# Kernel tuning notes

Measured on AMD Instinct MI355X. Metric: run time of the kernel, lower is better.

The kernel has to match this reference:

```python
import jax, jax.numpy as jnp
import numpy as np

T, B, V, E, H, L = 128, 32, 50000, 512, 512, 2


def _lstm_layer(x, h0, c0, Wih, Whh, bih, bhh):
    # x: [T, B, in]; torch gate order i, f, g, o
    def step(carry, xt):
        h, c = carry
        gates = xt @ Wih.T + bih + h @ Whh.T + bhh  # [B, 4H]
        i, f, g, o = jnp.split(gates, 4, axis=-1)
        c = jax.nn.sigmoid(f) * c + jax.nn.sigmoid(i) * jnp.tanh(g)
        h = jax.nn.sigmoid(o) * jnp.tanh(c)
        return (h, c), h
    (h, c), ys = jax.lax.scan(step, (h0, c0), x)
    return ys, h, c


def setup_inputs() -> dict:
    key = jax.random.key(0)
    ks = jax.random.split(key, 12)
    s = 0.02
    return {
        'word': jax.random.randint(ks[0], (B,), 0, V),
        'seq': jax.random.randint(ks[1], (T, B), 0, V),
        'emb': jax.random.normal(ks[2], (V, E), jnp.float32) * s,
        'w2h_W': jax.random.normal(ks[3], (H, E), jnp.float32) * s,
        'w2h_b': jnp.zeros((H,), jnp.float32),
        'Wih0': jax.random.normal(ks[4], (4 * H, E), jnp.float32) * s,
        'Whh0': jax.random.normal(ks[5], (4 * H, H), jnp.float32) * s,
        'bih0': jnp.zeros((4 * H,), jnp.float32),
        'bhh0': jnp.zeros((4 * H,), jnp.float32),
        'Wih1': jax.random.normal(ks[6], (4 * H, H), jnp.float32) * s,
        'Whh1': jax.random.normal(ks[7], (4 * H, H), jnp.float32) * s,
        'bih1': jnp.zeros((4 * H,), jnp.float32),
        'bhh1': jnp.zeros((4 * H,), jnp.float32),
        'dec_W': jax.random.normal(ks[8], (V, H), jnp.float32) * s,
        'dec_b': jnp.zeros((V,), jnp.float32),
    }


def reference(word, seq, emb, w2h_W, w2h_b, Wih0, Whh0, bih0, bhh0,
              Wih1, Whh1, bih1, bhh1, dec_W, dec_b):
    word_emb = emb[word]                       # [B, E]
    seq_emb = emb[seq]                         # [T, B, E] (dropouts are 0/eval)
    # init_hidden: c0 = word2hidden(word_emb) expanded to all layers, h0 = 0
    c0 = word_emb @ w2h_W.T + w2h_b            # [B, H]
    h0 = jnp.zeros_like(c0)
    # 2-layer LSTM; stepping all layers per timestep == running layers sequentially
    y0, h_f0, c_f0 = _lstm_layer(seq_emb, h0, c0, Wih0, Whh0, bih0, bhh0)
    y1, h_f1, c_f1 = _lstm_layer(y0, h0, c0, Wih1, Whh1, bih1, bhh1)
    out = y1.reshape(T * B, H)                 # [T*B, H]
    decoded = out @ dec_W.T + dec_b            # [T*B, V]
    h_final = jnp.stack([h_f0, h_f1], axis=0)  # [L, B, H]
    c_final = jnp.stack([c_f0, c_f1], axis=0)
    return decoded, h_final, c_final
```

## Files before the change

### kernel.cpp

```cpp
#include <hip/hip_runtime.h>
#include <hip/hip_bf16.h>
#include <cstdint>

#define T_STEPS 128
#define BATCH   32
#define VOCAB   50000
#define EDIM    512
#define HDIM    512
#define GDIM    2048
#define MROWS   4096
#define VPAD    50048
#define BH      (BATCH * HDIM)
#define CONV_BLOCKS 224

typedef short bf16x8 __attribute__((ext_vector_type(8)));
typedef float f32x4  __attribute__((ext_vector_type(4)));
typedef unsigned short us4 __attribute__((ext_vector_type(4)));
typedef unsigned short us8 __attribute__((ext_vector_type(8)));

#define MFMA16(a, b, c) __builtin_amdgcn_mfma_f32_16x16x32_bf16(a, b, c, 0, 0, 0)

__device__ __forceinline__ float fsigmoid(float x) {
    return 1.0f / (1.0f + __expf(-x));
}
__device__ __forceinline__ float ftanh(float x) {
    return 1.0f - 2.0f / (1.0f + __expf(2.0f * x));
}

__device__ __forceinline__ unsigned short f2bf(float f) {
    unsigned int u = __float_as_uint(f);
    u = (u + 0x7fffu + ((u >> 16) & 1u)) >> 16;
    return (unsigned short)u;
}


__global__ __launch_bounds__(64) void pack_all(const float* __restrict__ s0,
                                               const float* __restrict__ s1,
                                               const float* __restrict__ s2,
                                               const float* __restrict__ s3,
                                               unsigned short* __restrict__ d0,
                                               unsigned short* __restrict__ d1,
                                               unsigned short* __restrict__ d2,
                                               unsigned short* __restrict__ d3) {
    const int which = blockIdx.x >> 11;
    const int n = blockIdx.x & 2047;
    const float* src = (which == 0) ? s0 : (which == 1) ? s1 : (which == 2) ? s2 : s3;
    unsigned short* dst = (which == 0) ? d0 : (which == 1) ? d1 : (which == 2) ? d2 : d3;
    const int orig = (n & 3) * 512 + (n >> 2);
    const int k = threadIdx.x * 8;
    const float* s = src + (long)orig * 512 + k;
    float4 a = *(const float4*)s;
    float4 b = *(const float4*)(s + 4);
    us8 v;
    v[0] = f2bf(a.x); v[1] = f2bf(a.y); v[2] = f2bf(a.z); v[3] = f2bf(a.w);
    v[4] = f2bf(b.x); v[5] = f2bf(b.y); v[6] = f2bf(b.z); v[7] = f2bf(b.w);
    *(us8*)(dst + (long)n * 512 + k) = v;
}

__global__ __launch_bounds__(256) void pack_bias(const float* __restrict__ bih0,
                                                 const float* __restrict__ bhh0,
                                                 const float* __restrict__ bih1,
                                                 const float* __restrict__ bhh1,
                                                 float* __restrict__ b0p,
                                                 float* __restrict__ b1p) {
    const int n = blockIdx.x * 256 + threadIdx.x;
    const int orig = (n & 3) * 512 + (n >> 2);
    b0p[n] = bih0[orig] + bhh0[orig];
    b1p[n] = bih1[orig] + bhh1[orig];
}

__global__ __launch_bounds__(256) void gather_x(const int* __restrict__ seq,
                                                const float* __restrict__ emb,
                                                unsigned short* __restrict__ Xbf) {
    long i = ((long)blockIdx.x * 256 + threadIdx.x) * 4;
    if (i >= (long)MROWS * EDIM) return;
    int r   = (int)(i >> 9);
    int col = (int)(i & 511);
    const float* er = emb + (long)seq[r] * EDIM + col;
    float4 e = *(const float4*)er;
    us4 v;
    v[0] = f2bf(e.x); v[1] = f2bf(e.y); v[2] = f2bf(e.z); v[3] = f2bf(e.w);
    *(us4*)(Xbf + i) = v;
}

__global__ __launch_bounds__(256) void init_c0(const int* __restrict__ word,
                                               const float* __restrict__ emb,
                                               const float* __restrict__ w2hW,
                                               const float* __restrict__ w2hb,
                                               float* __restrict__ c0s, float* __restrict__ c1s,
                                               unsigned short* __restrict__ y0bf,
                                               unsigned short* __restrict__ y1bf) {
    const int idx = blockIdx.x * 256 + threadIdx.x;
    const int b = idx >> 9, hh = idx & 511;
    const float* er = emb + (long)word[b] * EDIM;
    const float* wr = w2hW + (long)hh * EDIM;
    float acc = w2hb[hh];
    #pragma unroll 4
    for (int k = 0; k < EDIM; k += 4) {
        float4 e4 = *(const float4*)(er + k);
        float4 w4 = *(const float4*)(wr + k);
        acc += e4.x * w4.x + e4.y * w4.y + e4.z * w4.z + e4.w * w4.w;
    }
    c0s[idx] = acc;
    c1s[idx] = acc;
    y0bf[idx] = 0;
    y1bf[idx] = 0;
}

__global__ __launch_bounds__(256) void gemm_bt128(const unsigned short* __restrict__ A,
                                                  const unsigned short* __restrict__ Bt,
                                                  float* __restrict__ C,
                                                  const float* __restrict__ bias1,
                                                  const float* __restrict__ bias2,
                                                  int K, int Nreal, long ldc, int ntn,
                                                  int banded) {
    __shared__ __align__(16) unsigned char smem[34048];
    unsigned short* As = (unsigned short*)smem;
    unsigned short* Bs = (unsigned short*)(smem + 16384);
    float* ctile = (float*)smem;

    const int tid  = threadIdx.x;
    long m0, n0;
    if (banded) {
        const int band  = blockIdx.x / 736;
        const int local = blockIdx.x % 736;
        m0 = (long)(local / 23) * 128;
        n0 = (long)(band * 23 + local % 23) * 128;
    } else {
        m0 = (long)(blockIdx.x / ntn) * 128;
        n0 = (long)(blockIdx.x % ntn) * 128;
    }
    const int lane = tid & 63;
    const int wave = tid >> 6;
    const int wr = wave >> 1, wc = wave & 1;
    const int fr = lane & 15, fq = lane >> 4;

    f32x4 acc[4][4];
    #pragma unroll
    for (int i = 0; i < 4; ++i)
        #pragma unroll
        for (int j = 0; j < 4; ++j) acc[i][j] = (f32x4)0.0f;

    const int srow = tid >> 3;
    const int scol = (tid & 7) * 8;

    for (int kt = 0; kt < K; kt += 64) {
        #pragma unroll
        for (int i = 0; i < 4; ++i) {
            const unsigned short* ga = A  + (m0 + i * 32 + srow) * K + kt + scol;
            const unsigned short* gb = Bt + (n0 + i * 32 + srow) * K + kt + scol;
            __builtin_amdgcn_global_load_lds((const __attribute__((address_space(1))) void*)ga,
                                             (__attribute__((address_space(3))) void*)(As + i * 2048 + tid * 8),
                                             16, 0, 0);
            __builtin_amdgcn_global_load_lds((const __attribute__((address_space(1))) void*)gb,
                                             (__attribute__((address_space(3))) void*)(Bs + i * 2048 + tid * 8),
                                             16, 0, 0);
        }
        asm volatile("s_waitcnt vmcnt(0)" ::: "memory");
        __syncthreads();
        #pragma unroll
        for (int ks = 0; ks < 64; ks += 32) {
            bf16x8 af[4], bfr[4];
            #pragma unroll
            for (int mi = 0; mi < 4; ++mi)
                af[mi] = *(const bf16x8*)&As[(wr * 64 + mi * 16 + fr) * 64 + ks + fq * 8];
            #pragma unroll
            for (int ni = 0; ni < 4; ++ni)
                bfr[ni] = *(const bf16x8*)&Bs[(wc * 64 + ni * 16 + fr) * 64 + ks + fq * 8];
            #pragma unroll
            for (int mi = 0; mi < 4; ++mi)
                #pragma unroll
                for (int ni = 0; ni < 4; ++ni)
                    acc[mi][ni] = MFMA16(af[mi], bfr[ni], acc[mi][ni]);
        }
        __syncthreads();
    }

    #pragma unroll
    for (int h = 0; h < 2; ++h) {
        if (wr == h) {
            #pragma unroll
            for (int ni = 0; ni < 4; ++ni) {
                const long col = n0 + wc * 64 + ni * 16 + fr;
                float bs = 0.0f;
                if (col < Nreal)
                    bs = (bias1 ? bias1[col] : 0.0f) + (bias2 ? bias2[col] : 0.0f);
                #pragma unroll
                for (int mi = 0; mi < 4; ++mi)
                    #pragma unroll
                    for (int r = 0; r < 4; ++r)
                        ctile[(mi * 16 + fq * 4 + r) * 132 + wc * 64 + ni * 16 + fr] =
                            acc[mi][ni][r] + bs;
            }
        }
        __syncthreads();
        #pragma unroll
        for (int j = 0; j < 8; ++j) {
            const int flat = tid + j * 256;
            const int row = flat >> 5, colq = flat & 31;
            const long col4 = n0 + colq * 4;
            if (col4 < Nreal) {
                f32x4 v = *(const f32x4*)&ctile[row * 132 + colq * 4];
                *(f32x4*)&C[(m0 + h * 64 + row) * ldc + col4] = v;
            }
        }
        __syncthreads();
    }
}

__global__ __launch_bounds__(512) void lstm_step2(
        const float* __restrict__ G0,
        const unsigned short* __restrict__ Whh0p,
        const unsigned short* __restrict__ Wih1p,
        const unsigned short* __restrict__ Whh1p,
        const float* __restrict__ b1p,
        unsigned short* __restrict__ y0bf,
        unsigned short* __restrict__ y1bf,
        float* __restrict__ c0s, float* __restrict__ c1s,
        float* __restrict__ hf,
        const float* __restrict__ decW,
        unsigned short* __restrict__ decWb,
        int t) {
    __shared__ float part[8][32][32];
    int bid = blockIdx.x;
    const int tid  = threadIdx.x;

    if (bid >= 128) {
        const long cid = (long)(bid - 128) + (long)t * CONV_BLOCKS;
        const long i = (cid * 512 + tid) * 8;
        if (i >= (long)VPAD * EDIM) return;
        const long row = i >> 9;
        us8 v;
        if (row < VOCAB) {
            float4 a = *(const float4*)(decW + i);
            float4 b = *(const float4*)(decW + i + 4);
            v[0] = f2bf(a.x); v[1] = f2bf(a.y); v[2] = f2bf(a.z); v[3] = f2bf(a.w);
            v[4] = f2bf(b.x); v[5] = f2bf(b.y); v[6] = f2bf(b.z); v[7] = f2bf(b.w);
        } else {
            v = (us8)0;
        }
        *(us8*)(decWb + i) = v;
        return;
    }

    const int wv   = tid >> 6, lane = tid & 63;
    const int fr   = lane & 15, fq = lane >> 4;

    int layer, tt, cg;
    if (bid < 64) { layer = 0; tt = t;     if (tt >= T_STEPS) return; cg = bid; }
    else          { layer = 1; tt = t - 1; if (tt < 0) return;       cg = bid - 64; }

    const unsigned short* hin;
    unsigned short* yout;
    float* cs;
    if (layer == 0) { hin = y0bf + (long)tt * BH; yout = y0bf + (long)(tt + 1) * BH; cs = c0s; }
    else            { hin = y1bf + (long)tt * BH; yout = y1bf + (long)(tt + 1) * BH; cs = c1s; }

    const int n_base = cg * 32;

    const int pb = tid >> 3, pu = tid & 7;
    const int si = pb * HDIM + cg * 8 + pu;
    float creg = 0.0f;
    float4 ad = make_float4(0.f, 0.f, 0.f, 0.f);
    if (tid < 256) {
        creg = cs[si];
        if (layer == 0) ad = *(const float4*)(G0 + ((long)tt * BATCH + pb) * GDIM + n_base + pu * 4);
        else            ad = *(const float4*)(b1p + n_base + pu * 4);
    }

    f32x4 acc[2][2];
    acc[0][0] = (f32x4)0.0f; acc[0][1] = (f32x4)0.0f;
    acc[1][0] = (f32x4)0.0f; acc[1][1] = (f32x4)0.0f;

    if (layer == 0) {
        const int kbase = wv * 64;
        const unsigned short* A0 = hin + fr * 512 + kbase + fq * 8;
        const unsigned short* A1 = A0 + 16 * 512;
        const unsigned short* B0 = Whh0p + (long)(n_base + fr) * 512 + kbase + fq * 8;
        const unsigned short* B1 = B0 + 16 * 512;
        #pragma unroll
        for (int i = 0; i < 2; ++i) {
            bf16x8 a0 = *(const bf16x8*)(A0 + i * 32);
            bf16x8 a1 = *(const bf16x8*)(A1 + i * 32);
            bf16x8 b0 = *(const bf16x8*)(B0 + i * 32);
            bf16x8 b1 = *(const bf16x8*)(B1 + i * 32);
            acc[0][0] = MFMA16(a0, b0, acc[0][0]);
            acc[0][1] = MFMA16(a0, b1, acc[0][1]);
            acc[1][0] = MFMA16(a1, b0, acc[1][0]);
            acc[1][1] = MFMA16(a1, b1, acc[1][1]);
        }
    } else {
        const unsigned short* Aop = (wv < 4) ? (y0bf + (long)(tt + 1) * BH) : hin;
        const unsigned short* Bop = (wv < 4) ? Wih1p : Whh1p;
        const int kbase = (wv & 3) * 128;
        const unsigned short* A0 = Aop + fr * 512 + kbase + fq * 8;
        const unsigned short* A1 = A0 + 16 * 512;
        const unsigned short* B0 = Bop + (long)(n_base + fr) * 512 + kbase + fq * 8;
        const unsigned short* B1 = B0 + 16 * 512;
        #pragma unroll
        for (int i = 0; i < 4; ++i) {
            bf16x8 a0 = *(const bf16x8*)(A0 + i * 32);
            bf16x8 a1 = *(const bf16x8*)(A1 + i * 32);
            bf16x8 b0 = *(const bf16x8*)(B0 + i * 32);
            bf16x8 b1 = *(const bf16x8*)(B1 + i * 32);
            acc[0][0] = MFMA16(a0, b0, acc[0][0]);
            acc[0][1] = MFMA16(a0, b1, acc[0][1]);
            acc[1][0] = MFMA16(a1, b0, acc[1][0]);
            acc[1][1] = MFMA16(a1, b1, acc[1][1]);
        }
    }

    #pragma unroll
    for (int mi = 0; mi < 2; ++mi)
        #pragma unroll
        for (int ni = 0; ni < 2; ++ni)
            #pragma unroll
            for (int r = 0; r < 4; ++r)
                part[wv][mi * 16 + fq * 4 + r][ni * 16 + fr] = acc[mi][ni][r];
    __syncthreads();

    if (tid < 256) {
        float4 g4 = *(const float4*)&part[0][pb][pu * 4];
        #pragma unroll
        for (int w = 1; w < 8; ++w) {
            float4 p4 = *(const float4*)&part[w][pb][pu * 4];
            g4.x += p4.x; g4.y += p4.y; g4.z += p4.z; g4.w += p4.w;
        }
        const float vi = g4.x + ad.x, vf = g4.y + ad.y;
        const float vg = g4.z + ad.z, vo = g4.w + ad.w;
        float c = fsigmoid(vf) * creg + fsigmoid(vi) * ftanh(vg);
        float h = fsigmoid(vo) * ftanh(c);
        cs[si] = c;
        yout[si] = f2bf(h);
        if (tt == T_STEPS - 1) hf[layer * BH + si] = h;
    }
}

__global__ __launch_bounds__(256) void finalize_states(const float* __restrict__ hf,
                                                       const float* __restrict__ c0s,
                                                       const float* __restrict__ c1s,
                                                       float* __restrict__ out) {
    const int idx = blockIdx.x * 256 + threadIdx.x;
    const long base = (long)MROWS * VOCAB;
    float v;
    if (idx < 32768)      v = hf[idx];
    else if (idx < 49152) v = c0s[idx - 32768];
    else                  v = c1s[idx - 49152];
    out[base + idx] = v;
}

extern "C" void kernel_launch(void* const* d_in, const int* in_sizes, int n_in,
                              void* d_out, int out_size, void* d_ws, size_t ws_size,
                              hipStream_t stream) {
    const int*   word  = (const int*)d_in[0];
    const int*   seq   = (const int*)d_in[1];
    const float* emb   = (const float*)d_in[2];
    const float* w2hW  = (const float*)d_in[3];
    const float* w2hb  = (const float*)d_in[4];
    const float* Wih0  = (const float*)d_in[5];
    const float* Whh0  = (const float*)d_in[6];
    const float* bih0  = (const float*)d_in[7];
    const float* bhh0  = (const float*)d_in[8];
    const float* Wih1  = (const float*)d_in[9];
    const float* Whh1  = (const float*)d_in[10];
    const float* bih1  = (const float*)d_in[11];
    const float* bhh1  = (const float*)d_in[12];
    const float* dec_W = (const float*)d_in[13];
    const float* dec_b = (const float*)d_in[14];
    float* out = (float*)d_out;

    char* ws = (char*)d_ws;
    size_t off = 0;
    float*          G0    = (float*)(ws + off);          off += (size_t)MROWS * GDIM * 4;
    unsigned short* Xbf   = (unsigned short*)(ws + off); off += (size_t)MROWS * EDIM * 2;
    unsigned short* Wih0p = (unsigned short*)(ws + off); off += (size_t)GDIM  * EDIM * 2;
    unsigned short* Whh0p = (unsigned short*)(ws + off); off += (size_t)GDIM  * HDIM * 2;
    unsigned short* Wih1p = (unsigned short*)(ws + off); off += (size_t)GDIM  * HDIM * 2;
    unsigned short* Whh1p = (unsigned short*)(ws + off); off += (size_t)GDIM  * HDIM * 2;
    unsigned short* decWb = (unsigned short*)(ws + off); off += (size_t)VPAD  * EDIM * 2;
    unsigned short* y0bf  = (unsigned short*)(ws + off); off += (size_t)(T_STEPS + 1) * BH * 2;
    unsigned short* y1bf  = (unsigned short*)(ws + off); off += (size_t)(T_STEPS + 1) * BH * 2;
    float* b0p = (float*)(ws + off); off += (size_t)GDIM * 4;
    float* b1p = (float*)(ws + off); off += (size_t)GDIM * 4;
    float* c0s = (float*)(ws + off); off += (size_t)BH * 4;
    float* c1s = (float*)(ws + off); off += (size_t)BH * 4;
    float* hf  = (float*)(ws + off); off += (size_t)2 * BH * 4;

    pack_all<<<4 * 2048, 64, 0, stream>>>(Wih0, Whh0, Wih1, Whh1,
                                          Wih0p, Whh0p, Wih1p, Whh1p);
    pack_bias<<<8, 256, 0, stream>>>(bih0, bhh0, bih1, bhh1, b0p, b1p);
    gather_x<<<2048, 256, 0, stream>>>(seq, emb, Xbf);
    init_c0<<<64, 256, 0, stream>>>(word, emb, w2hW, w2hb, c0s, c1s, y0bf, y1bf);

    gemm_bt128<<<32 * 16, 256, 0, stream>>>(Xbf, Wih0p, G0, b0p, nullptr,
                                            512, GDIM, (long)GDIM, 16, 0);

    for (int t = 0; t <= T_STEPS; ++t)
        lstm_step2<<<128 + CONV_BLOCKS, 512, 0, stream>>>(
            G0, Whh0p, Wih1p, Whh1p, b1p, y0bf, y1bf, c0s, c1s, hf,
            dec_W, decWb, t);

    gemm_bt128<<<32 * 391, 256, 0, stream>>>(y1bf + BH, decWb, out, dec_b, nullptr,
                                             512, VOCAB, (long)VOCAB, 391, 1);

    finalize_states<<<256, 256, 0, stream>>>(hf, c0s, c1s, out);
}
```

Before: 1.375 ms.

## Overlap decoder GEMM tiles with LSTM recurrence steps as y1 rows complete

Result: slower. 1.954 ms (+42.2%).

```diff
diff --git a/kernel.cpp b/kernel.cpp
--- a/kernel.cpp
+++ b/kernel.cpp
@@ -11,7 +11,9 @@
 #define MROWS   4096
 #define VPAD    50048
 #define BH      (BATCH * HDIM)
-#define CONV_BLOCKS 224
+#define NTILE_N 782
+#define NTILES_TOT (32 * NTILE_N)
+#define FUSED_TILES 24046
 
 typedef short bf16x8 __attribute__((ext_vector_type(8)));
 typedef float f32x4  __attribute__((ext_vector_type(4)));
@@ -20,12 +22,8 @@
 
 #define MFMA16(a, b, c) __builtin_amdgcn_mfma_f32_16x16x32_bf16(a, b, c, 0, 0, 0)
 
-__device__ __forceinline__ float fsigmoid(float x) {
-    return 1.0f / (1.0f + __expf(-x));
-}
-__device__ __forceinline__ float ftanh(float x) {
-    return 1.0f - 2.0f / (1.0f + __expf(2.0f * x));
-}
+__device__ __forceinline__ float fsigmoid(float x) { return 1.0f / (1.0f + __expf(-x)); }
+__device__ __forceinline__ float ftanh(float x)    { return 1.0f - 2.0f / (1.0f + __expf(2.0f * x)); }
 
 __device__ __forceinline__ unsigned short f2bf(float f) {
     unsigned int u = __float_as_uint(f);
@@ -111,25 +109,35 @@
                                                   const unsigned short* __restrict__ Bt,
                                                   float* __restrict__ C,
                                                   const float* __restrict__ bias1,
-                                                  const float* __restrict__ bias2,
                                                   int K, int Nreal, long ldc, int ntn,
-                                                  int banded) {
+                                                  const float* __restrict__ cvsrc,
+                                                  unsigned short* __restrict__ cvdst,
+                                                  int ngemm) {
+    const int tid  = threadIdx.x;
+    if (blockIdx.x >= ngemm) {
+        long i = ((long)(blockIdx.x - ngemm) * 256 + tid) * 8;
+        if (i >= (long)VPAD * EDIM) return;
+        long row = i >> 9;
+        us8 v;
+        if (row < VOCAB) {
+            float4 a = *(const float4*)(cvsrc + i);
+            float4 b = *(const float4*)(cvsrc + i + 4);
+            v[0] = f2bf(a.x); v[1] = f2bf(a.y); v[2] = f2bf(a.z); v[3] = f2bf(a.w);
+            v[4] = f2bf(b.x); v[5] = f2bf(b.y); v[6] = f2bf(b.z); v[7] = f2bf(b.w);
+        } else {
+            v = (us8)0;
+        }
+        *(us8*)(cvdst + i) = v;
+        return;
+    }
+
     __shared__ __align__(16) unsigned char smem[34048];
     unsigned short* As = (unsigned short*)smem;
     unsigned short* Bs = (unsigned short*)(smem + 16384);
     float* ctile = (float*)smem;
 
-    const int tid  = threadIdx.x;
-    long m0, n0;
-    if (banded) {
-        const int band  = blockIdx.x / 736;
-        const int local = blockIdx.x % 736;
-        m0 = (long)(local / 23) * 128;
-        n0 = (long)(band * 23 + local % 23) * 128;
-    } else {
-        m0 = (long)(blockIdx.x / ntn) * 128;
-        n0 = (long)(blockIdx.x % ntn) * 128;
-    }
+    const long m0  = (long)(blockIdx.x / ntn) * 128;
+    const long n0  = (long)(blockIdx.x % ntn) * 128;
     const int lane = tid & 63;
     const int wave = tid >> 6;
     const int wr = wave >> 1, wc = wave & 1;
@@ -182,9 +190,7 @@
             #pragma unroll
             for (int ni = 0; ni < 4; ++ni) {
                 const long col = n0 + wc * 64 + ni * 16 + fr;
-                float bs = 0.0f;
-                if (col < Nreal)
-                    bs = (bias1 ? bias1[col] : 0.0f) + (bias2 ? bias2[col] : 0.0f);
+                float bs = (col < Nreal && bias1) ? bias1[col] : 0.0f;
                 #pragma unroll
                 for (int mi = 0; mi < 4; ++mi)
                     #pragma unroll
@@ -202,6 +208,89 @@
             if (col4 < Nreal) {
                 f32x4 v = *(const f32x4*)&ctile[row * 132 + colq * 4];
                 *(f32x4*)&C[(m0 + h * 64 + row) * ldc + col4] = v;
+            }
+        }
+        __syncthreads();
+    }
+}
+
+__device__ __forceinline__ void decode_tile(int tau,
+                                            const unsigned short* __restrict__ y1A,
+                                            const unsigned short* __restrict__ decWb,
+                                            const float* __restrict__ dec_b,
+                                            float* __restrict__ out,
+                                            char* smem, int tid) {
+    unsigned short* As = (unsigned short*)smem;
+    unsigned short* Bs = (unsigned short*)(smem + 16384);
+    float* ctile = (float*)smem;
+
+    const int mi = tau / NTILE_N, nj = tau % NTILE_N;
+    const long m0 = (long)mi * 128, n0 = (long)nj * 64;
+    const int srow = tid >> 3, scol = (tid & 7) * 8;
+    const int wv = tid >> 6, lane = tid & 63;
+    const int wr = wv >> 1, wc = wv & 1;
+    const int fr = lane & 15, fq = lane >> 4;
+
+    f32x4 acc[2][2];
+    acc[0][0] = (f32x4)0.0f; acc[0][1] = (f32x4)0.0f;
+    acc[1][0] = (f32x4)0.0f; acc[1][1] = (f32x4)0.0f;
+
+    for (int kt = 0; kt < 512; kt += 64) {
+        #pragma unroll
+        for (int i = 0; i < 2; ++i) {
+            const unsigned short* ga = y1A + (m0 + i * 64 + srow) * 512 + kt + scol;
+            __builtin_amdgcn_global_load_lds((const __attribute__((address_space(1))) void*)ga,
+                                             (__attribute__((address_space(3))) void*)(As + i * 4096 + tid * 8),
+                                             16, 0, 0);
+        }
+        const unsigned short* gb = decWb + (n0 + srow) * 512 + kt + scol;
+        __builtin_amdgcn_global_load_lds((const __attribute__((address_space(1))) void*)gb,
+                                         (__attribute__((address_space(3))) void*)(Bs + tid * 8),
+                                         16, 0, 0);
+        asm volatile("s_waitcnt vmcnt(0)" ::: "memory");
+        __syncthreads();
+        #pragma unroll
+        for (int ks = 0; ks < 64; ks += 32) {
+            bf16x8 af[2], bfr[2];
+            #pragma unroll
+            for (int m2 = 0; m2 < 2; ++m2)
+                af[m2] = *(const bf16x8*)&As[(wr * 32 + m2 * 16 + fr) * 64 + ks + fq * 8];
+            #pragma unroll
+            for (int n2 = 0; n2 < 2; ++n2)
+                bfr[n2] = *(const bf16x8*)&Bs[(wc * 32 + n2 * 16 + fr) * 64 + ks + fq * 8];
+            #pragma unroll
+            for (int m2 = 0; m2 < 2; ++m2)
+                #pragma unroll
+                for (int n2 = 0; n2 < 2; ++n2)
+                    acc[m2][n2] = MFMA16(af[m2], bfr[n2], acc[m2][n2]);
+        }
+        __syncthreads();
+    }
+
+    #pragma unroll
+    for (int h = 0; h < 2; ++h) {
+        if ((wr >> 1) == h) {
+            #pragma unroll
+            for (int n2 = 0; n2 < 2; ++n2) {
+                const long col = n0 + wc * 32 + n2 * 16 + fr;
+                float bs = (col < VOCAB) ? dec_b[col] : 0.0f;
+                #pragma unroll
+                for (int m2 = 0; m2 < 2; ++m2)
+                    #pragma unroll
+                    for (int r = 0; r < 4; ++r)
+                        ctile[((wr & 1) * 32 + m2 * 16 + fq * 4 + r) * 68 + wc * 32 + n2 * 16 + fr] =
+                            acc[m2][n2][r] + bs;
+            }
+        }
+        __syncthreads();
+        #pragma unroll
+        for (int j = 0; j < 2; ++j) {
+            const int flat = tid + j * 512;
+            const int row = flat >> 4, colq = flat & 15;
+            const long col4 = n0 + colq * 4;
+            if (col4 < VOCAB) {
+                f32x4 v = *(const f32x4*)&ctile[row * 68 + colq * 4];
+                *(f32x4*)&out[(m0 + h * 64 + row) * (long)VOCAB + col4] = v;
             }
         }
         __syncthreads();
@@ -218,31 +307,20 @@
         unsigned short* __restrict__ y1bf,
         float* __restrict__ c0s, float* __restrict__ c1s,
         float* __restrict__ hf,
-        const float* __restrict__ decW,
-        unsigned short* __restrict__ decWb,
-        int t) {
-    __shared__ float part[8][32][32];
+        const unsigned short* __restrict__ decWb,
+        const float* __restrict__ dec_b,
+        float* __restrict__ out,
+        int t, int sd) {
+    __shared__ __align__(16) char smem[32768];
     int bid = blockIdx.x;
     const int tid  = threadIdx.x;
 
     if (bid >= 128) {
-        const long cid = (long)(bid - 128) + (long)t * CONV_BLOCKS;
-        const long i = (cid * 512 + tid) * 8;
-        if (i >= (long)VPAD * EDIM) return;
-        const long row = i >> 9;
-        us8 v;
-        if (row < VOCAB) {
-            float4 a = *(const float4*)(decW + i);
-            float4 b = *(const float4*)(decW + i + 4);
-            v[0] = f2bf(a.x); v[1] = f2bf(a.y); v[2] = f2bf(a.z); v[3] = f2bf(a.w);
-            v[4] = f2bf(b.x); v[5] = f2bf(b.y); v[6] = f2bf(b.z); v[7] = f2bf(b.w);
-        } else {
-            v = (us8)0;
-        }
-        *(us8*)(decWb + i) = v;
+        decode_tile(sd + bid - 128, y1bf + BH, decWb, dec_b, out, smem, tid);
         return;
     }
 
+    float (*part)[32][32] = (float(*)[32][32])smem;
     const int wv   = tid >> 6, lane = tid & 63;
     const int fr   = lane & 15, fq = lane >> 4;
 
@@ -334,6 +412,14 @@
         yout[si] = f2bf(h);
         if (tt == T_STEPS - 1) hf[layer * BH + si] = h;
     }
+}
+
+__global__ __launch_bounds__(512) void decode_tail(const unsigned short* __restrict__ y1bf,
+                                                   const unsigned short* __restrict__ decWb,
+                                                   const float* __restrict__ dec_b,
+                                                   float* __restrict__ out, int tau0) {
+    __shared__ __align__(16) char smem[32768];
+    decode_tile(tau0 + blockIdx.x, y1bf + BH, decWb, dec_b, out, smem, threadIdx.x);
 }
 
 __global__ __launch_bounds__(256) void finalize_states(const float* __restrict__ hf,
@@ -392,16 +478,25 @@
     gather_x<<<2048, 256, 0, stream>>>(seq, emb, Xbf);
     init_c0<<<64, 256, 0, stream>>>(word, emb, w2hW, w2hb, c0s, c1s, y0bf, y1bf);
 
-    gemm_bt128<<<32 * 16, 256, 0, stream>>>(Xbf, Wih0p, G0, b0p, nullptr,
-                                            512, GDIM, (long)GDIM, 16, 0);
-
-    for (int t = 0; t <= T_STEPS; ++t)
-        lstm_step2<<<128 + CONV_BLOCKS, 512, 0, stream>>>(
+    gemm_bt128<<<512 + 12512, 256, 0, stream>>>(Xbf, Wih0p, G0, b0p,
+                                                512, GDIM, (long)GDIM, 16,
+                                                dec_W, decWb, 512);
+
+    auto S = [](int d) -> int {
+        if (d <= 6) return 0;
+        long v = (long)NTILE_N * (d - 6) / 4;
+        return (v > FUSED_TILES) ? FUSED_TILES : (int)v;
+    };
+
+    for (int t = 0; t <= T_STEPS; ++t) {
+        const int sd = S(t), ntiles = S(t + 1) - sd;
+        lstm_step2<<<128 + ntiles, 512, 0, stream>>>(
             G0, Whh0p, Wih1p, Whh1p, b1p, y0bf, y1bf, c0s, c1s, hf,
-            dec_W, decWb, t);
-
-    gemm_bt128<<<32 * 391, 256, 0, stream>>>(y1bf + BH, decWb, out, dec_b, nullptr,
-                                             512, VOCAB, (long)VOCAB, 391, 1);
+            decWb, dec_b, out, t, sd);
+    }
+
+    decode_tail<<<NTILES_TOT - FUSED_TILES, 512, 0, stream>>>(y1bf, decWb, dec_b,
+                                                              out, FUSED_TILES);
 
     finalize_states<<<256, 256, 0, stream>>>(hf, c0s, c1s, out);
 }
```

## Move decoder weight conversion into input GEMM and double-buffer GEMM LDS loads

Applied to the files above, without the earlier changes.

New measurement: 1.364 ms. No clear change (-0.8%).

```diff
diff --git a/kernel.cpp b/kernel.cpp
--- a/kernel.cpp
+++ b/kernel.cpp
@@ -11,7 +11,6 @@
 #define MROWS   4096
 #define VPAD    50048
 #define BH      (BATCH * HDIM)
-#define CONV_BLOCKS 224
 
 typedef short bf16x8 __attribute__((ext_vector_type(8)));
 typedef float f32x4  __attribute__((ext_vector_type(4)));
@@ -20,12 +19,8 @@
 
 #define MFMA16(a, b, c) __builtin_amdgcn_mfma_f32_16x16x32_bf16(a, b, c, 0, 0, 0)
 
-__device__ __forceinline__ float fsigmoid(float x) {
-    return 1.0f / (1.0f + __expf(-x));
-}
-__device__ __forceinline__ float ftanh(float x) {
-    return 1.0f - 2.0f / (1.0f + __expf(2.0f * x));
-}
+__device__ __forceinline__ float fsigmoid(float x) { return 1.0f / (1.0f + __expf(-x)); }
+__device__ __forceinline__ float ftanh(float x)    { return 1.0f - 2.0f / (1.0f + __expf(2.0f * x)); }
 
 __device__ __forceinline__ unsigned short f2bf(float f) {
     unsigned int u = __float_as_uint(f);
@@ -111,29 +106,39 @@
                                                   const unsigned short* __restrict__ Bt,
                                                   float* __restrict__ C,
                                                   const float* __restrict__ bias1,
-                                                  const float* __restrict__ bias2,
                                                   int K, int Nreal, long ldc, int ntn,
-                                                  int banded) {
-    __shared__ __align__(16) unsigned char smem[34048];
-    unsigned short* As = (unsigned short*)smem;
-    unsigned short* Bs = (unsigned short*)(smem + 16384);
+                                                  const float* __restrict__ cvsrc,
+                                                  unsigned short* __restrict__ cvdst,
+                                                  int ngemm) {
+    const int tid  = threadIdx.x;
+    if (blockIdx.x >= ngemm) {
+        long i = ((long)(blockIdx.x - ngemm) * 256 + tid) * 8;
+        if (i >= (long)VPAD * EDIM) return;
+        long row = i >> 9;
+        us8 v;
+        if (row < VOCAB) {
+            float4 a = *(const float4*)(cvsrc + i);
+            float4 b = *(const float4*)(cvsrc + i + 4);
+            v[0] = f2bf(a.x); v[1] = f2bf(a.y); v[2] = f2bf(a.z); v[3] = f2bf(a.w);
+            v[4] = f2bf(b.x); v[5] = f2bf(b.y); v[6] = f2bf(b.z); v[7] = f2bf(b.w);
+        } else {
+            v = (us8)0;
+        }
+        *(us8*)(cvdst + i) = v;
+        return;
+    }
+
+    __shared__ __align__(16) unsigned char smem[65536];
     float* ctile = (float*)smem;
 
-    const int tid  = threadIdx.x;
-    long m0, n0;
-    if (banded) {
-        const int band  = blockIdx.x / 736;
-        const int local = blockIdx.x % 736;
-        m0 = (long)(local / 23) * 128;
-        n0 = (long)(band * 23 + local % 23) * 128;
-    } else {
-        m0 = (long)(blockIdx.x / ntn) * 128;
-        n0 = (long)(blockIdx.x % ntn) * 128;
-    }
+    const long m0  = (long)(blockIdx.x / ntn) * 128;
+    const long n0  = (long)(blockIdx.x % ntn) * 128;
     const int lane = tid & 63;
     const int wave = tid >> 6;
     const int wr = wave >> 1, wc = wave & 1;
     const int fr = lane & 15, fq = lane >> 4;
+    const int srow = tid >> 3;
+    const int scol = (tid & 7) * 8;
 
     f32x4 acc[4][4];
     #pragma unroll
@@ -141,10 +146,9 @@
         #pragma unroll
         for (int j = 0; j < 4; ++j) acc[i][j] = (f32x4)0.0f;
 
-    const int srow = tid >> 3;
-    const int scol = (tid & 7) * 8;
-
-    for (int kt = 0; kt < K; kt += 64) {
+    auto issue = [&](int kt, int b) {
+        unsigned short* As = (unsigned short*)(smem + (b << 15));
+        unsigned short* Bs = (unsigned short*)(smem + (b << 15) + 16384);
         #pragma unroll
         for (int i = 0; i < 4; ++i) {
             const unsigned short* ga = A  + (m0 + i * 32 + srow) * K + kt + scol;
@@ -156,17 +160,30 @@
                                              (__attribute__((address_space(3))) void*)(Bs + i * 2048 + tid * 8),
                                              16, 0, 0);
         }
-        asm volatile("s_waitcnt vmcnt(0)" ::: "memory");
+    };
+
+    const int NK = K >> 6;
+    issue(0, 0);
+    for (int k = 0; k < NK; ++k) {
+        const int cur = k & 1;
+        if (k + 1 < NK) {
+            issue((k + 1) << 6, cur ^ 1);
+            asm volatile("s_waitcnt vmcnt(8)" ::: "memory");
+        } else {
+            asm volatile("s_waitcnt vmcnt(0)" ::: "memory");
+        }
         __syncthreads();
+        const unsigned short* Asc = (const unsigned short*)(smem + (cur << 15));
+        const unsigned short* Bsc = (const unsigned short*)(smem + (cur << 15) + 16384);
         #pragma unroll
         for (int ks = 0; ks < 64; ks += 32) {
             bf16x8 af[4], bfr[4];
             #pragma unroll
             for (int mi = 0; mi < 4; ++mi)
-                af[mi] = *(const bf16x8*)&As[(wr * 64 + mi * 16 + fr) * 64 + ks + fq * 8];
+                af[mi] = *(const bf16x8*)&Asc[(wr * 64 + mi * 16 + fr) * 64 + ks + fq * 8];
             #pragma unroll
             for (int ni = 0; ni < 4; ++ni)
-                bfr[ni] = *(const bf16x8*)&Bs[(wc * 64 + ni * 16 + fr) * 64 + ks + fq * 8];
+                bfr[ni] = *(const bf16x8*)&Bsc[(wc * 64 + ni * 16 + fr) * 64 + ks + fq * 8];
             #pragma unroll
             for (int mi = 0; mi < 4; ++mi)
                 #pragma unroll
@@ -182,9 +199,7 @@
             #pragma unroll
             for (int ni = 0; ni < 4; ++ni) {
                 const long col = n0 + wc * 64 + ni * 16 + fr;
-                float bs = 0.0f;
-                if (col < Nreal)
-                    bs = (bias1 ? bias1[col] : 0.0f) + (bias2 ? bias2[col] : 0.0f);
+                float bs = (col < Nreal && bias1) ? bias1[col] : 0.0f;
                 #pragma unroll
                 for (int mi = 0; mi < 4; ++mi)
                     #pragma unroll
@@ -218,31 +233,10 @@
         unsigned short* __restrict__ y1bf,
         float* __restrict__ c0s, float* __restrict__ c1s,
         float* __restrict__ hf,
-        const float* __restrict__ decW,
-        unsigned short* __restrict__ decWb,
         int t) {
     __shared__ float part[8][32][32];
     int bid = blockIdx.x;
     const int tid  = threadIdx.x;
-
-    if (bid >= 128) {
-        const long cid = (long)(bid - 128) + (long)t * CONV_BLOCKS;
-        const long i = (cid * 512 + tid) * 8;
-        if (i >= (long)VPAD * EDIM) return;
-        const long row = i >> 9;
-        us8 v;
-        if (row < VOCAB) {
-            float4 a = *(const float4*)(decW + i);
-            float4 b = *(const float4*)(decW + i + 4);
-            v[0] = f2bf(a.x); v[1] = f2bf(a.y); v[2] = f2bf(a.z); v[3] = f2bf(a.w);
-            v[4] = f2bf(b.x); v[5] = f2bf(b.y); v[6] = f2bf(b.z); v[7] = f2bf(b.w);
-        } else {
-            v = (us8)0;
-        }
-        *(us8*)(decWb + i) = v;
-        return;
-    }
-
     const int wv   = tid >> 6, lane = tid & 63;
     const int fr   = lane & 15, fq = lane >> 4;
 
@@ -392,16 +386,17 @@
     gather_x<<<2048, 256, 0, stream>>>(seq, emb, Xbf);
     init_c0<<<64, 256, 0, stream>>>(word, emb, w2hW, w2hb, c0s, c1s, y0bf, y1bf);
 
-    gemm_bt128<<<32 * 16, 256, 0, stream>>>(Xbf, Wih0p, G0, b0p, nullptr,
-                                            512, GDIM, (long)GDIM, 16, 0);
+    gemm_bt128<<<512 + 12512, 256, 0, stream>>>(Xbf, Wih0p, G0, b0p,
+                                                512, GDIM, (long)GDIM, 16,
+                                                dec_W, decWb, 512);
 
     for (int t = 0; t <= T_STEPS; ++t)
-        lstm_step2<<<128 + CONV_BLOCKS, 512, 0, stream>>>(
-            G0, Whh0p, Wih1p, Whh1p, b1p, y0bf, y1bf, c0s, c1s, hf,
-            dec_W, decWb, t);
-
-    gemm_bt128<<<32 * 391, 256, 0, stream>>>(y1bf + BH, decWb, out, dec_b, nullptr,
-                                             512, VOCAB, (long)VOCAB, 391, 1);
+        lstm_step2<<<128, 512, 0, stream>>>(G0, Whh0p, Wih1p, Whh1p, b1p,
+                                            y0bf, y1bf, c0s, c1s, hf, t);
+
+    gemm_bt128<<<32 * 391, 256, 0, stream>>>(y1bf + BH, decWb, out, dec_b,
+                                             512, VOCAB, (long)VOCAB, 391,
+                                             nullptr, nullptr, 32 * 391);
 
     finalize_states<<<256, 256, 0, stream>>>(hf, c0s, c1s, out);
 }
```
